# Performance work log

Measured on AMD Instinct MI355X. Metric: run time of the kernel, lower is better.

The kernel has to match this reference:

```python
import jax, jax.numpy as jnp
import numpy as np

H = 4      # attention heads
C = 64     # hidden_dim per head
GAT_SLOPE = 0.2   # PyG GATConv leaky_relu negative_slope
ACT_SLOPE = 0.01  # nn.LeakyReLU / F.leaky_relu default


def gat_layer(x, src, dst, W, a_src, a_dst, b, n):
    # x: [n, F_in] -> h: [n, H, C]
    h = (x @ W).reshape(n, H, C)
    al_s = jnp.einsum('nhc,hc->nh', h, a_src)  # [n, H]
    al_d = jnp.einsum('nhc,hc->nh', h, a_dst)
    e = jax.nn.leaky_relu(al_s[src] + al_d[dst], GAT_SLOPE)  # [E, H]
    # segment softmax over destination nodes (self-loops ensure non-empty segments)
    m = jax.ops.segment_max(e, dst, num_segments=n)
    p = jnp.exp(e - m[dst])
    s = jax.ops.segment_sum(p, dst, num_segments=n)
    alpha = p / s[dst]
    out = jax.ops.segment_sum(h[src] * alpha[:, :, None], dst, num_segments=n)  # [n, H, C]
    return out.reshape(n, H * C) + b


def setup_inputs() -> dict:
    key = jax.random.key(0)
    ks = jax.random.split(key, 24)
    N, E = 102400, 409600
    F_IN, F_OUT = 80, 80
    HC = H * C
    RIN, RHID, ROUT = 60, 512, 60
    def g(k, shape, scale):
        return (jax.random.normal(k, shape, dtype=jnp.float32) * scale)
    inp = {
        'x': g(ks[0], (N, F_IN), 1.0),
        'edge_index': jax.random.randint(ks[1], (2, E), 0, N, dtype=jnp.int64),
        'root_ctx_norm': g(ks[2], (4096, RIN), 1.0),
        'W0': g(ks[3], (F_IN, HC), 0.1), 'a_src0': g(ks[4], (H, C), 0.1), 'a_dst0': g(ks[5], (H, C), 0.1), 'b0': jnp.zeros((HC,), jnp.float32),
        'W1': g(ks[6], (HC, HC), 0.06), 'a_src1': g(ks[7], (H, C), 0.1), 'a_dst1': g(ks[8], (H, C), 0.1), 'b1': jnp.zeros((HC,), jnp.float32),
        'W2': g(ks[9], (HC, HC), 0.06), 'a_src2': g(ks[10], (H, C), 0.1), 'a_dst2': g(ks[11], (H, C), 0.1), 'b2': jnp.zeros((HC,), jnp.float32),
        'fc_w': g(ks[12], (HC, F_OUT), 0.06), 'fc_b': jnp.zeros((F_OUT,), jnp.float32),
        'r_w1': g(ks[13], (RIN, RHID), 0.1), 'r_b1': jnp.zeros((RHID,), jnp.float32),
        'r_w2': g(ks[14], (RHID, RHID), 0.04), 'r_b2': jnp.zeros((RHID,), jnp.float32),
        'r_w3': g(ks[15], (RHID, ROUT), 0.04), 'r_b3': jnp.zeros((ROUT,), jnp.float32),
    }
    return inp


def reference(x, edge_index, root_ctx_norm,
              W0, a_src0, a_dst0, b0,
              W1, a_src1, a_dst1, b1,
              W2, a_src2, a_dst2, b2,
              fc_w, fc_b, r_w1, r_b1, r_w2, r_b2, r_w3, r_b3):
    n = x.shape[0]
    loops = jnp.arange(n, dtype=edge_index.dtype)
    src = jnp.concatenate([edge_index[0], loops])  # PyG add_self_loops=True
    dst = jnp.concatenate([edge_index[1], loops])
    h = gat_layer(x, src, dst, W0, a_src0, a_dst0, b0, n)
    h = jax.nn.leaky_relu(h, ACT_SLOPE)  # dropout is identity in eval
    h = gat_layer(h, src, dst, W1, a_src1, a_dst1, b1, n)
    h = jax.nn.leaky_relu(h, ACT_SLOPE)
    h = gat_layer(h, src, dst, W2, a_src2, a_dst2, b2, n)
    rot = h @ fc_w + fc_b
    r = jax.nn.leaky_relu(root_ctx_norm @ r_w1 + r_b1, ACT_SLOPE)
    r = jax.nn.leaky_relu(r @ r_w2 + r_b2, ACT_SLOPE)
    root_norm = r @ r_w3 + r_b3
    return rot, root_norm
```

## Files before the change

kernel.cpp:

```cpp
#include <hip/hip_runtime.h>
#include <hip/hip_bf16.h>


#define GAT_SLOPE 0.2f
#define ACT_SLOPE 0.01f

typedef unsigned short ushort_t;
typedef __attribute__((ext_vector_type(8))) short bf16x8;
typedef __attribute__((ext_vector_type(8))) unsigned short ushort8v;
typedef __attribute__((ext_vector_type(4))) float floatx4;

__device__ __forceinline__ float lrelu(float x, float s) {
    return fmaxf(x, s * x);
}

__device__ __forceinline__ ushort_t f2bf(float f) {
    union { float f; unsigned u; } x; x.f = f;
    unsigned r = x.u + 0x7FFF + ((x.u >> 16) & 1);
    return (ushort_t)(r >> 16);
}

__device__ __forceinline__ float bf2f(ushort_t u) {
    union { unsigned u; float f; } x; x.u = ((unsigned)u) << 16;
    return x.f;
}

__global__ void detect_fmt(const int* __restrict__ raw, int nwords, int* flag) {
    __shared__ int nz;
    if (threadIdx.x == 0) nz = 0;
    __syncthreads();
    int lim = nwords < 4096 ? nwords : 4096;
    for (int i = threadIdx.x * 2 + 1; i < lim; i += 512)
        if (raw[i] != 0) atomicAdd(&nz, 1);
    __syncthreads();
    if (threadIdx.x == 0) *flag = (nz == 0) ? 1 : 0;
}

__global__ void zero2(int* __restrict__ a, int* __restrict__ b, int n) {
    int i = blockIdx.x * blockDim.x + threadIdx.x;
    if (i < n) { a[i] = 0; b[i] = 0; }
}

__global__ void convert_count(const int* __restrict__ raw, int E,
                              const int* __restrict__ flag,
                              int* __restrict__ idx32, int* __restrict__ counts) {
    int i = blockIdx.x * blockDim.x + threadIdx.x;
    if (i >= E) return;
    int f = *flag;
    int s = f ? raw[2 * i] : raw[i];
    int d = f ? raw[2 * (E + i)] : raw[E + i];
    idx32[i] = s;
    idx32[E + i] = d;
    atomicAdd(&counts[d], 1);
}

__global__ void scan_block(const int* __restrict__ counts, int* __restrict__ inc,
                           int* __restrict__ blockSums, int N) {
    __shared__ int sh[256];
    int i = blockIdx.x * 256 + threadIdx.x;
    int v = (i < N) ? counts[i] : 0;
    sh[threadIdx.x] = v;
    __syncthreads();
    for (int off = 1; off < 256; off <<= 1) {
        int t = (threadIdx.x >= off) ? sh[threadIdx.x - off] : 0;
        __syncthreads();
        sh[threadIdx.x] += t;
        __syncthreads();
    }
    if (i < N) inc[i] = sh[threadIdx.x];
    if (threadIdx.x == 255) blockSums[blockIdx.x] = sh[255];
}

__global__ void scan_sums(int* __restrict__ blockSums, int nb, int* __restrict__ row_ptr) {
    __shared__ int sh[512];
    int v = ((int)threadIdx.x < nb) ? blockSums[threadIdx.x] : 0;
    sh[threadIdx.x] = v;
    __syncthreads();
    for (int off = 1; off < 512; off <<= 1) {
        int t = (threadIdx.x >= off) ? sh[threadIdx.x - off] : 0;
        __syncthreads();
        sh[threadIdx.x] += t;
        __syncthreads();
    }
    if ((int)threadIdx.x < nb) blockSums[threadIdx.x] = sh[threadIdx.x];
    if (threadIdx.x == 0) row_ptr[0] = 0;
}

__global__ void scan_add(const int* __restrict__ inc, const int* __restrict__ blockSums,
                         int* __restrict__ row_ptr, int N) {
    int i = blockIdx.x * 256 + threadIdx.x;
    if (i < N) row_ptr[i + 1] = inc[i] + (blockIdx.x > 0 ? blockSums[blockIdx.x - 1] : 0);
}

__global__ void edge_fill(const int* __restrict__ src, const int* __restrict__ dst, int E,
                          const int* __restrict__ row_ptr, int* __restrict__ cursor,
                          int* __restrict__ col) {
    int i = blockIdx.x * blockDim.x + threadIdx.x;
    if (i < E) {
        int d = dst[i];
        int pos = row_ptr[d] + atomicAdd(&cursor[d], 1);
        col[pos] = src[i];
    }
}

__global__ void convert_padrow(const float* __restrict__ in, ushort_t* __restrict__ out,
                               int M, int Kr, int Kp) {
    int i = blockIdx.x * blockDim.x + threadIdx.x;
    if (i >= M * Kp) return;
    int r = i / Kp, c = i - r * Kp;
    out[i] = f2bf((c < Kr) ? in[(size_t)r * Kr + c] : 0.f);
}

struct WConv { const float* in; ushort_t* out; int Kp, Kr, N, Npad, blkOff; };
struct WConvArr { WConv e[7]; int n; };

__global__ void convert_w_multi(WConvArr a) {
    int b = blockIdx.x;
    int ei = 0;
    for (int k = 1; k < a.n; k++)
        if (b >= a.e[k].blkOff) ei = k;
    WConv w = a.e[ei];
    int i = (b - w.blkOff) * 256 + threadIdx.x;
    if (i >= w.Npad * w.Kp) return;
    int n = i / w.Kp, k = i - n * w.Kp;
    float v = (n < w.N && k < w.Kr) ? w.in[(size_t)k * w.N + n] : 0.f;
    w.out[i] = f2bf(v);
}

#define LOADR(tt)                                     \
    do {                                              \
        int k0_ = (tt) << 5;                          \
        rA0 = *(const ushort8v*)(gA0 + k0_);          \
        rA1 = *(const ushort8v*)(gA1 + k0_);          \
        rB0 = *(const ushort8v*)(gB0 + k0_);          \
        rB1 = *(const ushort8v*)(gB1 + k0_);          \
    } while (0)

#define WRITER(b)                                     \
    do {                                              \
        *(ushort8v*)(&As[b][wsl0]) = rA0;             \
        *(ushort8v*)(&As[b][wsl1]) = rA1;             \
        *(ushort8v*)(&Bs[b][wsl0]) = rB0;             \
        *(ushort8v*)(&Bs[b][wsl1]) = rB1;             \
    } while (0)

#define GEMM_PIPELINE(NT)                                                        \
    ushort8v rA0, rA1, rB0, rB1;                                                 \
    LOADR(0);                                                                    \
    WRITER(0);                                                                   \
    LOADR(1);                                                                    \
    asm volatile("s_waitcnt lgkmcnt(0)" ::: "memory");                           \
    __builtin_amdgcn_s_barrier();                                                \
    for (int kt = 0; kt < (NT); ++kt) {                                          \
        int b = kt & 1;                                                          \
        if (kt + 1 < (NT)) WRITER(b ^ 1);                                        \
        if (kt + 2 < (NT)) LOADR(kt + 2);                                        \
        bf16x8 af[4], bfv[4];                                                    \
        _Pragma("unroll")                                                        \
        for (int i = 0; i < 4; i++)                                              \
            af[i] = *(const bf16x8*)(&As[b][(wm + i * 16 + lrow) * 32            \
                                            + lquad * 8]);                       \
        _Pragma("unroll")                                                        \
        for (int j = 0; j < 4; j++)                                              \
            bfv[j] = *(const bf16x8*)(&Bs[b][(wn + j * 16 + lrow) * 32           \
                                             + lquad * 8]);                      \
        _Pragma("unroll")                                                        \
        for (int i = 0; i < 4; i++)                                              \
            _Pragma("unroll")                                                    \
            for (int j = 0; j < 4; j++)                                          \
                acc[i][j] = __builtin_amdgcn_mfma_f32_16x16x32_bf16(             \
                    af[i], bfv[j], acc[i][j], 0, 0, 0);                          \
        asm volatile("s_waitcnt lgkmcnt(0)" ::: "memory");                       \
        __builtin_amdgcn_s_barrier();                                            \
    }

__global__ __launch_bounds__(256) void gemm_gat(
    const ushort_t* __restrict__ A, const ushort_t* __restrict__ Bt,
    const float* __restrict__ a_src, const float* __restrict__ a_dst,
    ushort_t* __restrict__ Hbf, float* __restrict__ al_s, float* __restrict__ al_d,
    int K, int auxY,
    const ushort_t* __restrict__ xA, const ushort_t* __restrict__ xBt,
    const float* __restrict__ xBias, void* __restrict__ xC,
    int xN, int xK, int xGX, int xCnt, int xAct, float xSlope, int xOutBf) {
    __shared__ __align__(16) ushort_t As[2][128 * 32];
    __shared__ __align__(16) ushort_t Bs[2][128 * 32];
    int t = threadIdx.x;
    int wave = t >> 6, lane = t & 63;
    int wm = (wave >> 1) << 6;
    int wn = (wave & 1) << 6;
    int lrow = lane & 15, lquad = lane >> 4;
    const int wsl0 = (wave * 64 + lane) * 8;
    const int wsl1 = (256 + wave * 64 + lane) * 8;
    int c0 = wave * 64 + lane;
    int c1 = 256 + c0;

    floatx4 acc[4][4];
#pragma unroll
    for (int i = 0; i < 4; i++)
#pragma unroll
        for (int j = 0; j < 4; j++) acc[i][j] = (floatx4){0.f, 0.f, 0.f, 0.f};

    if ((int)blockIdx.y >= auxY) {
        int rowBase = (blockIdx.y - auxY) << 7;
        int colBase = blockIdx.x << 7;
        const ushort_t* gA0 = A + (size_t)(rowBase + (c0 >> 2)) * K + ((c0 & 3) << 3);
        const ushort_t* gB0 = Bt + (size_t)(colBase + (c0 >> 2)) * K + ((c0 & 3) << 3);
        const ushort_t* gA1 = A + (size_t)(rowBase + (c1 >> 2)) * K + ((c1 & 3) << 3);
        const ushort_t* gB1 = Bt + (size_t)(colBase + (c1 >> 2)) * K + ((c1 & 3) << 3);
        const int nt = K >> 5;
        GEMM_PIPELINE(nt);

        int head = (colBase + wn) >> 6;
        float avs[4], avd[4];
#pragma unroll
        for (int j = 0; j < 4; j++) {
            avs[j] = a_src[head * 64 + j * 16 + lrow];
            avd[j] = a_dst[head * 64 + j * 16 + lrow];
        }
#pragma unroll
        for (int i = 0; i < 4; i++) {
#pragma unroll
            for (int r = 0; r < 4; r++) {
                float ps = 0.f, pd = 0.f;
#pragma unroll
                for (int j = 0; j < 4; j++) {
                    ps += acc[i][j][r] * avs[j];
                    pd += acc[i][j][r] * avd[j];
                }
#pragma unroll
                for (int off = 1; off < 16; off <<= 1) {
                    ps += __shfl_xor(ps, off);
                    pd += __shfl_xor(pd, off);
                }
                if (lrow == 0) {
                    int gr = rowBase + wm + i * 16 + lquad * 4 + r;
                    al_s[gr * 4 + head] = ps;
                    al_d[gr * 4 + head] = pd;
                }
            }
            int grb = rowBase + wm + i * 16 + lquad * 4;
#pragma unroll
            for (int j = 0; j < 4; j++) {
                int gc = colBase + wn + j * 16 + lrow;
#pragma unroll
                for (int r = 0; r < 4; r++)
                    Hbf[(size_t)(grb + r) * 256 + gc] = f2bf(acc[i][j][r]);
            }
        }
    } else {
        int id = blockIdx.y * 2 + blockIdx.x;
        if (id >= xCnt) return;
        int bxp = id % xGX, byp = id / xGX;
        int rowBase = byp << 7;
        int colBase = bxp << 7;
        const ushort_t* gA0 = xA + (size_t)(rowBase + (c0 >> 2)) * xK + ((c0 & 3) << 3);
        const ushort_t* gB0 = xBt + (size_t)(colBase + (c0 >> 2)) * xK + ((c0 & 3) << 3);
        const ushort_t* gA1 = xA + (size_t)(rowBase + (c1 >> 2)) * xK + ((c1 & 3) << 3);
        const ushort_t* gB1 = xBt + (size_t)(colBase + (c1 >> 2)) * xK + ((c1 & 3) << 3);
        const int nt = xK >> 5;
        GEMM_PIPELINE(nt);

#pragma unroll
        for (int i = 0; i < 4; i++) {
            int gr = rowBase + wm + i * 16 + lquad * 4;
#pragma unroll
            for (int j = 0; j < 4; j++) {
                int gc = colBase + wn + j * 16 + lrow;
                if (gc >= xN) continue;
                float b = xBias ? xBias[gc] : 0.f;
#pragma unroll
                for (int r = 0; r < 4; r++) {
                    float v = acc[i][j][r] + b;
                    if (xAct) v = lrelu(v, xSlope);
                    if (xOutBf)
                        ((ushort_t*)xC)[(size_t)(gr + r) * xN + gc] = f2bf(v);
                    else
                        ((float*)xC)[(size_t)(gr + r) * xN + gc] = v;
                }
            }
        }
    }
}

__global__ __launch_bounds__(256) void gemm_plain(
    const ushort_t* __restrict__ A, const ushort_t* __restrict__ Bt,
    const float* __restrict__ bias, void* __restrict__ Cout,
    int M, int N, int K, int act, float slope, int outBf) {
    __shared__ __align__(16) ushort_t As[2][128 * 32];
    __shared__ __align__(16) ushort_t Bs[2][128 * 32];
    int t = threadIdx.x;
    int wave = t >> 6, lane = t & 63;
    int wm = (wave >> 1) << 6;
    int wn = (wave & 1) << 6;
    int rowBase = blockIdx.y << 7;
    int colBase = blockIdx.x << 7;
    int lrow = lane & 15, lquad = lane >> 4;
    floatx4 acc[4][4];
#pragma unroll
    for (int i = 0; i < 4; i++)
#pragma unroll
        for (int j = 0; j < 4; j++) acc[i][j] = (floatx4){0.f, 0.f, 0.f, 0.f};

    int c0 = wave * 64 + lane;
    const ushort_t* gA0 = A + (size_t)(rowBase + (c0 >> 2)) * K + ((c0 & 3) << 3);
    const ushort_t* gB0 = Bt + (size_t)(colBase + (c0 >> 2)) * K + ((c0 & 3) << 3);
    int c1 = 256 + c0;
    const ushort_t* gA1 = A + (size_t)(rowBase + (c1 >> 2)) * K + ((c1 & 3) << 3);
    const ushort_t* gB1 = Bt + (size_t)(colBase + (c1 >> 2)) * K + ((c1 & 3) << 3);
    const int wsl0 = (wave * 64 + lane) * 8;
    const int wsl1 = (256 + wave * 64 + lane) * 8;

    const int nt = K >> 5;
    GEMM_PIPELINE(nt);

#pragma unroll
    for (int i = 0; i < 4; i++) {
        int gr = rowBase + wm + i * 16 + lquad * 4;
#pragma unroll
        for (int j = 0; j < 4; j++) {
            int gc = colBase + wn + j * 16 + lrow;
            if (gc >= N) continue;
            float b = bias ? bias[gc] : 0.f;
#pragma unroll
            for (int r = 0; r < 4; r++) {
                float v = acc[i][j][r] + b;
                if (act) v = lrelu(v, slope);
                if (outBf)
                    ((ushort_t*)Cout)[(size_t)(gr + r) * N + gc] = f2bf(v);
                else
                    ((float*)Cout)[(size_t)(gr + r) * N + gc] = v;
            }
        }
    }
}

__global__ __launch_bounds__(256) void gat_agg(
    const ushort_t* __restrict__ h_bf, const float* __restrict__ al_s,
    const float* __restrict__ al_d, const int* __restrict__ row_ptr,
    const int* __restrict__ col, const float* __restrict__ bias,
    ushort_t* __restrict__ out_bf, int N, int act, float slope) {
    int wid = (blockIdx.x * 256 + threadIdx.x) >> 6;
    int lane = threadIdx.x & 63;
    int half = lane >> 5;
    int lane8 = lane & 31;
    int n = wid * 2 + half;
    if (n >= N) return;
    int head = lane8 >> 3;
    int idx4 = n * 4 + head;
    float ad = al_d[idx4];
    const ushort8v* h8 = (const ushort8v*)h_bf;
    float p = __expf(lrelu(al_s[idx4] + ad, GAT_SLOPE));
    ushort8v hv = h8[(size_t)n * 32 + lane8];
    float s = p;
    float acc[8];
#pragma unroll
    for (int c = 0; c < 8; c++) acc[c] = p * bf2f(hv[c]);
    int beg = row_ptr[n], end = row_ptr[n + 1];
    for (int i = beg; i < end; i += 4) {
        int cnt = end - i;
        int sn0 = col[i];
        int sn1 = (cnt > 1) ? col[i + 1] : sn0;
        int sn2 = (cnt > 2) ? col[i + 2] : sn0;
        int sn3 = (cnt > 3) ? col[i + 3] : sn0;
        ushort8v h0 = h8[(size_t)sn0 * 32 + lane8];
        ushort8v h1 = h8[(size_t)sn1 * 32 + lane8];
        ushort8v h2 = h8[(size_t)sn2 * 32 + lane8];
        ushort8v h3 = h8[(size_t)sn3 * 32 + lane8];
        float a0 = al_s[sn0 * 4 + head];
        float a1 = al_s[sn1 * 4 + head];
        float a2 = al_s[sn2 * 4 + head];
        float a3 = al_s[sn3 * 4 + head];
        float p0 = __expf(lrelu(a0 + ad, GAT_SLOPE));
#pragma unroll
        for (int c = 0; c < 8; c++) acc[c] += p0 * bf2f(h0[c]);
        s += p0;
        if (cnt > 1) {
            float p1 = __expf(lrelu(a1 + ad, GAT_SLOPE));
#pragma unroll
            for (int c = 0; c < 8; c++) acc[c] += p1 * bf2f(h1[c]);
            s += p1;
        }
        if (cnt > 2) {
            float p2 = __expf(lrelu(a2 + ad, GAT_SLOPE));
#pragma unroll
            for (int c = 0; c < 8; c++) acc[c] += p2 * bf2f(h2[c]);
            s += p2;
        }
        if (cnt > 3) {
            float p3 = __expf(lrelu(a3 + ad, GAT_SLOPE));
#pragma unroll
            for (int c = 0; c < 8; c++) acc[c] += p3 * bf2f(h3[c]);
            s += p3;
        }
    }
    float rs = 1.f / s;
    const float4* b4 = (const float4*)bias;
    float4 b0 = b4[lane8 * 2];
    float4 b1 = b4[lane8 * 2 + 1];
    float bv[8] = {b0.x, b0.y, b0.z, b0.w, b1.x, b1.y, b1.z, b1.w};
    ushort8v o;
#pragma unroll
    for (int c = 0; c < 8; c++) {
        float v = acc[c] * rs + bv[c];
        if (act) v = lrelu(v, slope);
        o[c] = f2bf(v);
    }
    ((ushort8v*)out_bf)[(size_t)n * 32 + lane8] = o;
}

extern "C" void kernel_launch(void* const* d_in, const int* in_sizes, int n_in,
                              void* d_out, int out_size, void* d_ws, size_t ws_size,
                              hipStream_t stream) {
    const float* x        = (const float*)d_in[0];
    const int*   rawEdge  = (const int*)d_in[1];
    const float* rootCtx  = (const float*)d_in[2];
    const float* W[3]     = {(const float*)d_in[3], (const float*)d_in[7], (const float*)d_in[11]};
    const float* aS[3]    = {(const float*)d_in[4], (const float*)d_in[8], (const float*)d_in[12]};
    const float* aD[3]    = {(const float*)d_in[5], (const float*)d_in[9], (const float*)d_in[13]};
    const float* bb[3]    = {(const float*)d_in[6], (const float*)d_in[10], (const float*)d_in[14]};
    const float* fc_w     = (const float*)d_in[15];
    const float* fc_b     = (const float*)d_in[16];
    const float* r_w1     = (const float*)d_in[17];
    const float* r_b1     = (const float*)d_in[18];
    const float* r_w2     = (const float*)d_in[19];
    const float* r_b2     = (const float*)d_in[20];
    const float* r_w3     = (const float*)d_in[21];
    const float* r_b3     = (const float*)d_in[22];

    const int N  = in_sizes[0] / 80;
    const int E  = in_sizes[1] / 2;
    const int R  = in_sizes[2] / 60;
    const int N4 = N * 4;

    float* outRot  = (float*)d_out;
    float* outRoot = (float*)d_out + (size_t)N * 80;

    size_t off = 0;
    auto carve = [&](size_t bytes) -> void* {
        off = (off + 255) & ~(size_t)255;
        void* p = (char*)d_ws + off;
        off += bytes;
        return p;
    };
    int*      flag      = (int*)carve(4);
    int*      idx32     = (int*)carve((size_t)2 * E * 4);
    int*      counts    = (int*)carve((size_t)N * 4);
    int*      cursor    = (int*)carve((size_t)N * 4);
    int*      row_ptr   = (int*)carve((size_t)(N + 1) * 4);
    int*      incArr    = (int*)carve((size_t)N * 4);
    int*      blockSums = (int*)carve(512 * 4);
    int*      colArr    = (int*)carve((size_t)E * 4);
    float*    al_s      = (float*)carve((size_t)N4 * 4);
    float*    al_d      = (float*)carve((size_t)N4 * 4);
    ushort_t* h_bf      = (ushort_t*)carve((size_t)N * 256 * 2);
    ushort_t* agg_bf    = (ushort_t*)carve((size_t)N * 256 * 2);
    ushort_t* x_bf      = (ushort_t*)carve((size_t)N * 96 * 2);
    ushort_t* rc_bf     = (ushort_t*)carve((size_t)R * 64 * 2);
    ushort_t* t1_bf     = (ushort_t*)carve((size_t)R * 512 * 2);
    ushort_t* t2_bf     = (ushort_t*)carve((size_t)R * 512 * 2);
    ushort_t* Wt0       = (ushort_t*)carve((size_t)256 * 96 * 2);
    ushort_t* Wt1       = (ushort_t*)carve((size_t)256 * 256 * 2);
    ushort_t* Wt2       = (ushort_t*)carve((size_t)256 * 256 * 2);
    ushort_t* fcWt      = (ushort_t*)carve((size_t)128 * 256 * 2);
    ushort_t* rW1t      = (ushort_t*)carve((size_t)512 * 64 * 2);
    ushort_t* rWt2      = (ushort_t*)carve((size_t)512 * 512 * 2);
    ushort_t* rWt3      = (ushort_t*)carve((size_t)128 * 512 * 2);

    const int nb = (N + 255) / 256;
    dim3 blk(256);

    detect_fmt<<<1, 256, 0, stream>>>(rawEdge, 2 * E, flag);
    zero2<<<(N + 255) / 256, blk, 0, stream>>>(counts, cursor, N);
    convert_count<<<(E + 255) / 256, blk, 0, stream>>>(rawEdge, E, flag, idx32, counts);
    const int* srcArr = idx32;
    const int* dstArr = idx32 + E;
    scan_block<<<nb, 256, 0, stream>>>(counts, incArr, blockSums, N);
    scan_sums<<<1, 512, 0, stream>>>(blockSums, nb, row_ptr);
    scan_add<<<nb, 256, 0, stream>>>(incArr, blockSums, row_ptr, N);
    edge_fill<<<(E + 255) / 256, blk, 0, stream>>>(srcArr, dstArr, E, row_ptr, cursor, colArr);

    {
        WConvArr wa;
        auto mk = [&](int i, const float* in, ushort_t* out, int Kp, int Kr, int Nn, int Npad,
                      int blkOff) {
            wa.e[i] = WConv{in, out, Kp, Kr, Nn, Npad, blkOff};
        };
        int boff = 0;
        auto nblk = [](int Npad, int Kp) { return (Npad * Kp + 255) / 256; };
        mk(0, W[0], Wt0, 96, 80, 256, 256, boff);   boff += nblk(256, 96);
        mk(1, W[1], Wt1, 256, 256, 256, 256, boff); boff += nblk(256, 256);
        mk(2, W[2], Wt2, 256, 256, 256, 256, boff); boff += nblk(256, 256);
        mk(3, fc_w, fcWt, 256, 256, 80, 128, boff); boff += nblk(128, 256);
        mk(4, r_w1, rW1t, 64, 60, 512, 512, boff);  boff += nblk(512, 64);
        mk(5, r_w2, rWt2, 512, 512, 512, 512, boff); boff += nblk(512, 512);
        mk(6, r_w3, rWt3, 512, 512, 60, 128, boff);  boff += nblk(128, 512);
        wa.n = 7;
        convert_w_multi<<<boff, blk, 0, stream>>>(wa);
    }
    convert_padrow<<<(N * 96 + 255) / 256, blk, 0, stream>>>(x, x_bf, N, 80, 96);
    convert_padrow<<<(R * 64 + 255) / 256, blk, 0, stream>>>(rootCtx, rc_bf, R, 60, 64);

    const int aggBlocks = (N / 2 + 3) / 4;
    const int yMain = N / 128;
    const ushort_t* curA = x_bf;
    int curK = 96;
    const int mlpGY = R / 128;
    for (int l = 0; l < 3; l++) {
        const ushort_t* xA  = (l == 0) ? rc_bf : (l == 1 ? t1_bf : t2_bf);
        const ushort_t* xBt = (l == 0) ? rW1t : (l == 1 ? rWt2 : rWt3);
        const float*    xB  = (l == 0) ? r_b1 : (l == 1 ? r_b2 : r_b3);
        void*           xC  = (l == 0) ? (void*)t1_bf : (l == 1 ? (void*)t2_bf : (void*)outRoot);
        int xN   = (l == 2) ? 60 : 512;
        int xK   = (l == 0) ? 64 : 512;
        int xGX  = (l == 2) ? 1 : 4;
        int xCnt = xGX * mlpGY;
        int xAct = (l == 2) ? 0 : 1;
        int xOutBf = (l == 2) ? 0 : 1;
        int auxY = (xCnt + 1) / 2;
        dim3 g1(2, yMain + auxY);
        gemm_gat<<<g1, blk, 0, stream>>>(curA, l == 0 ? Wt0 : (l == 1 ? Wt1 : Wt2),
                                         aS[l], aD[l], h_bf, al_s, al_d,
                                         curK, auxY,
                                         xA, xBt, xB, xC,
                                         xN, xK, xGX, xCnt, xAct, ACT_SLOPE, xOutBf);
        int act = (l < 2) ? 1 : 0;
        gat_agg<<<aggBlocks, blk, 0, stream>>>(h_bf, al_s, al_d, row_ptr,
                                               colArr, bb[l], agg_bf, N,
                                               act, ACT_SLOPE);
        curA = agg_bf;
        curK = 256;
    }

    {
        dim3 g(1, N / 128);
        gemm_plain<<<g, blk, 0, stream>>>(agg_bf, fcWt, fc_b, outRot, N, 80, 256,
                                          0, 0.f, 0);
    }
}
```

Before: 469.4 us.

## Fuse graph preprocessing and weight conversion into one cooperative kernel

Replaces the separate format-detect, zeroing, count, three-stage scan, edge fill and bf16 conversion kernels with a single cooperative kernel that uses grid-wide syncs between phases. This is meant to remove per-launch overhead and the idle gaps between many small dependent kernels. In exchange, the work runs on a fixed 1024-block grid with grid-stride loops and pays grid-sync latency. It also relies on all blocks being co-resident.

```diff
diff --git a/kernel.cpp b/kernel.cpp
--- a/kernel.cpp
+++ b/kernel.cpp
@@ -1,5 +1,8 @@
 #include <hip/hip_runtime.h>
 #include <hip/hip_bf16.h>
+#include <hip/hip_cooperative_groups.h>
+
+namespace cg = cooperative_groups;
 
 
 #define GAT_SLOPE 0.2f
@@ -25,106 +28,129 @@
     return x.f;
 }
 
-__global__ void detect_fmt(const int* __restrict__ raw, int nwords, int* flag) {
-    __shared__ int nz;
-    if (threadIdx.x == 0) nz = 0;
-    __syncthreads();
-    int lim = nwords < 4096 ? nwords : 4096;
-    for (int i = threadIdx.x * 2 + 1; i < lim; i += 512)
-        if (raw[i] != 0) atomicAdd(&nz, 1);
-    __syncthreads();
-    if (threadIdx.x == 0) *flag = (nz == 0) ? 1 : 0;
-}
-
-__global__ void zero2(int* __restrict__ a, int* __restrict__ b, int n) {
-    int i = blockIdx.x * blockDim.x + threadIdx.x;
-    if (i < n) { a[i] = 0; b[i] = 0; }
-}
-
-__global__ void convert_count(const int* __restrict__ raw, int E,
-                              const int* __restrict__ flag,
-                              int* __restrict__ idx32, int* __restrict__ counts) {
-    int i = blockIdx.x * blockDim.x + threadIdx.x;
-    if (i >= E) return;
-    int f = *flag;
-    int s = f ? raw[2 * i] : raw[i];
-    int d = f ? raw[2 * (E + i)] : raw[E + i];
-    idx32[i] = s;
-    idx32[E + i] = d;
-    atomicAdd(&counts[d], 1);
-}
-
-__global__ void scan_block(const int* __restrict__ counts, int* __restrict__ inc,
-                           int* __restrict__ blockSums, int N) {
+struct WConv { const float* in; ushort_t* out; int Kp, Kr, N, Npad; };
+
+struct PreArgs {
+    const int* rawEdge;
+    int E, N, R;
+    int* flag;
+    int* idx32;
+    int* counts;
+    int* cursor;
+    int* row_ptr;
+    int* incArr;
+    int* blockSums;
+    int* colArr;
+    const float* x;  ushort_t* x_bf;
+    const float* rc; ushort_t* rc_bf;
+    WConv w[7];
+};
+
+__global__ void preamble_all(PreArgs a) {
+    cg::grid_group grid = cg::this_grid();
+    const int tid  = blockIdx.x * blockDim.x + threadIdx.x;
+    const int nthr = gridDim.x * blockDim.x;
     __shared__ int sh[256];
-    int i = blockIdx.x * 256 + threadIdx.x;
-    int v = (i < N) ? counts[i] : 0;
-    sh[threadIdx.x] = v;
-    __syncthreads();
-    for (int off = 1; off < 256; off <<= 1) {
-        int t = (threadIdx.x >= off) ? sh[threadIdx.x - off] : 0;
+
+    for (int i = tid; i < a.N; i += nthr) { a.counts[i] = 0; a.cursor[i] = 0; }
+    {
+        int tot = a.N * 96;
+        for (int i = tid; i < tot; i += nthr) {
+            int r = i / 96, c = i - r * 96;
+            a.x_bf[i] = f2bf((c < 80) ? a.x[(size_t)r * 80 + c] : 0.f);
+        }
+    }
+    {
+        int tot = a.R * 64;
+        for (int i = tid; i < tot; i += nthr) {
+            int r = i / 64, c = i - r * 64;
+            a.rc_bf[i] = f2bf((c < 60) ? a.rc[(size_t)r * 60 + c] : 0.f);
+        }
+    }
+    for (int e = 0; e < 7; e++) {
+        WConv w = a.w[e];
+        int tot = w.Npad * w.Kp;
+        for (int i = tid; i < tot; i += nthr) {
+            int n = i / w.Kp, k = i - n * w.Kp;
+            float v = (n < w.N && k < w.Kr) ? w.in[(size_t)k * w.N + n] : 0.f;
+            w.out[i] = f2bf(v);
+        }
+    }
+    if (blockIdx.x == 0) {
+        __shared__ int nz;
+        if (threadIdx.x == 0) nz = 0;
         __syncthreads();
-        sh[threadIdx.x] += t;
+        int lim = 2 * a.E < 4096 ? 2 * a.E : 4096;
+        for (int i = threadIdx.x * 2 + 1; i < lim; i += 512)
+            if (a.rawEdge[i] != 0) atomicAdd(&nz, 1);
         __syncthreads();
-    }
-    if (i < N) inc[i] = sh[threadIdx.x];
-    if (threadIdx.x == 255) blockSums[blockIdx.x] = sh[255];
-}
-
-__global__ void scan_sums(int* __restrict__ blockSums, int nb, int* __restrict__ row_ptr) {
-    __shared__ int sh[512];
-    int v = ((int)threadIdx.x < nb) ? blockSums[threadIdx.x] : 0;
-    sh[threadIdx.x] = v;
-    __syncthreads();
-    for (int off = 1; off < 512; off <<= 1) {
-        int t = (threadIdx.x >= off) ? sh[threadIdx.x - off] : 0;
+        if (threadIdx.x == 0) *a.flag = (nz == 0) ? 1 : 0;
+    }
+    grid.sync();
+
+    {
+        int fmt = *a.flag;
+        for (int i = tid; i < a.E; i += nthr) {
+            int s = fmt ? a.rawEdge[2 * i] : a.rawEdge[i];
+            int d = fmt ? a.rawEdge[2 * (a.E + i)] : a.rawEdge[a.E + i];
+            a.idx32[i] = s;
+            a.idx32[a.E + i] = d;
+            atomicAdd(&a.counts[d], 1);
+        }
+    }
+    grid.sync();
+
+    const int nb = (a.N + 255) / 256;
+    for (int ch = blockIdx.x; ch < nb; ch += gridDim.x) {
+        int i = ch * 256 + threadIdx.x;
+        int v = (i < a.N) ? a.counts[i] : 0;
+        sh[threadIdx.x] = v;
         __syncthreads();
-        sh[threadIdx.x] += t;
+        for (int off = 1; off < 256; off <<= 1) {
+            int t2 = (threadIdx.x >= off) ? sh[threadIdx.x - off] : 0;
+            __syncthreads();
+            sh[threadIdx.x] += t2;
+            __syncthreads();
+        }
+        if (i < a.N) a.incArr[i] = sh[threadIdx.x];
+        if (threadIdx.x == 255) a.blockSums[ch] = sh[255];
         __syncthreads();
     }
-    if ((int)threadIdx.x < nb) blockSums[threadIdx.x] = sh[threadIdx.x];
-    if (threadIdx.x == 0) row_ptr[0] = 0;
-}
-
-__global__ void scan_add(const int* __restrict__ inc, const int* __restrict__ blockSums,
-                         int* __restrict__ row_ptr, int N) {
-    int i = blockIdx.x * 256 + threadIdx.x;
-    if (i < N) row_ptr[i + 1] = inc[i] + (blockIdx.x > 0 ? blockSums[blockIdx.x - 1] : 0);
-}
-
-__global__ void edge_fill(const int* __restrict__ src, const int* __restrict__ dst, int E,
-                          const int* __restrict__ row_ptr, int* __restrict__ cursor,
-                          int* __restrict__ col) {
-    int i = blockIdx.x * blockDim.x + threadIdx.x;
-    if (i < E) {
-        int d = dst[i];
-        int pos = row_ptr[d] + atomicAdd(&cursor[d], 1);
-        col[pos] = src[i];
-    }
-}
-
-__global__ void convert_padrow(const float* __restrict__ in, ushort_t* __restrict__ out,
-                               int M, int Kr, int Kp) {
-    int i = blockIdx.x * blockDim.x + threadIdx.x;
-    if (i >= M * Kp) return;
-    int r = i / Kp, c = i - r * Kp;
-    out[i] = f2bf((c < Kr) ? in[(size_t)r * Kr + c] : 0.f);
-}
-
-struct WConv { const float* in; ushort_t* out; int Kp, Kr, N, Npad, blkOff; };
-struct WConvArr { WConv e[7]; int n; };
-
-__global__ void convert_w_multi(WConvArr a) {
-    int b = blockIdx.x;
-    int ei = 0;
-    for (int k = 1; k < a.n; k++)
-        if (b >= a.e[k].blkOff) ei = k;
-    WConv w = a.e[ei];
-    int i = (b - w.blkOff) * 256 + threadIdx.x;
-    if (i >= w.Npad * w.Kp) return;
-    int n = i / w.Kp, k = i - n * w.Kp;
-    float v = (n < w.N && k < w.Kr) ? w.in[(size_t)k * w.N + n] : 0.f;
-    w.out[i] = f2bf(v);
+    grid.sync();
+
+    if (blockIdx.x == 0) {
+        int carry = 0;
+        for (int base = 0; base < nb; base += 256) {
+            int idx = base + threadIdx.x;
+            int v = (idx < nb) ? a.blockSums[idx] : 0;
+            sh[threadIdx.x] = v;
+            __syncthreads();
+            for (int off = 1; off < 256; off <<= 1) {
+                int t2 = (threadIdx.x >= off) ? sh[threadIdx.x - off] : 0;
+                __syncthreads();
+                sh[threadIdx.x] += t2;
+                __syncthreads();
+            }
+            if (idx < nb) a.blockSums[idx] = sh[threadIdx.x] + carry;
+            int chunkTot = sh[255];
+            __syncthreads();
+            carry += chunkTot;
+        }
+    }
+    grid.sync();
+
+    for (int i = tid; i < a.N; i += nthr) {
+        int ch = i >> 8;
+        a.row_ptr[i + 1] = a.incArr[i] + (ch > 0 ? a.blockSums[ch - 1] : 0);
+    }
+    if (tid == 0) a.row_ptr[0] = 0;
+    grid.sync();
+
+    for (int i = tid; i < a.E; i += nthr) {
+        int d = a.idx32[a.E + i];
+        int pos = a.row_ptr[d] + atomicAdd(&a.cursor[d], 1);
+        a.colArr[pos] = a.idx32[i];
+    }
 }
 
 #define LOADR(tt)                                     \
@@ -464,41 +490,28 @@
     ushort_t* fcWt      = (ushort_t*)carve((size_t)128 * 256 * 2);
     ushort_t* rW1t      = (ushort_t*)carve((size_t)512 * 64 * 2);
     ushort_t* rWt2      = (ushort_t*)carve((size_t)512 * 512 * 2);
-    ushort_t* rWt3      = (ushort_t*)carve((size_t)128 * 512 * 2);
-
-    const int nb = (N + 255) / 256;
+    ushort_t* rWt3     = (ushort_t*)carve((size_t)128 * 512 * 2);
+
     dim3 blk(256);
 
-    detect_fmt<<<1, 256, 0, stream>>>(rawEdge, 2 * E, flag);
-    zero2<<<(N + 255) / 256, blk, 0, stream>>>(counts, cursor, N);
-    convert_count<<<(E + 255) / 256, blk, 0, stream>>>(rawEdge, E, flag, idx32, counts);
-    const int* srcArr = idx32;
-    const int* dstArr = idx32 + E;
-    scan_block<<<nb, 256, 0, stream>>>(counts, incArr, blockSums, N);
-    scan_sums<<<1, 512, 0, stream>>>(blockSums, nb, row_ptr);
-    scan_add<<<nb, 256, 0, stream>>>(incArr, blockSums, row_ptr, N);
-    edge_fill<<<(E + 255) / 256, blk, 0, stream>>>(srcArr, dstArr, E, row_ptr, cursor, colArr);
-
     {
-        WConvArr wa;
-        auto mk = [&](int i, const float* in, ushort_t* out, int Kp, int Kr, int Nn, int Npad,
-                      int blkOff) {
-            wa.e[i] = WConv{in, out, Kp, Kr, Nn, Npad, blkOff};
-        };
-        int boff = 0;
-        auto nblk = [](int Npad, int Kp) { return (Npad * Kp + 255) / 256; };
-        mk(0, W[0], Wt0, 96, 80, 256, 256, boff);   boff += nblk(256, 96);
-        mk(1, W[1], Wt1, 256, 256, 256, 256, boff); boff += nblk(256, 256);
-        mk(2, W[2], Wt2, 256, 256, 256, 256, boff); boff += nblk(256, 256);
-        mk(3, fc_w, fcWt, 256, 256, 80, 128, boff); boff += nblk(128, 256);
-        mk(4, r_w1, rW1t, 64, 60, 512, 512, boff);  boff += nblk(512, 64);
-        mk(5, r_w2, rWt2, 512, 512, 512, 512, boff); boff += nblk(512, 512);
-        mk(6, r_w3, rWt3, 512, 512, 60, 128, boff);  boff += nblk(128, 512);
-        wa.n = 7;
-        convert_w_multi<<<boff, blk, 0, stream>>>(wa);
-    }
-    convert_padrow<<<(N * 96 + 255) / 256, blk, 0, stream>>>(x, x_bf, N, 80, 96);
-    convert_padrow<<<(R * 64 + 255) / 256, blk, 0, stream>>>(rootCtx, rc_bf, R, 60, 64);
+        PreArgs pa;
+        pa.rawEdge = rawEdge; pa.E = E; pa.N = N; pa.R = R;
+        pa.flag = flag; pa.idx32 = idx32; pa.counts = counts; pa.cursor = cursor;
+        pa.row_ptr = row_ptr; pa.incArr = incArr; pa.blockSums = blockSums;
+        pa.colArr = colArr;
+        pa.x = x; pa.x_bf = x_bf; pa.rc = rootCtx; pa.rc_bf = rc_bf;
+        pa.w[0] = WConv{W[0], Wt0, 96, 80, 256, 256};
+        pa.w[1] = WConv{W[1], Wt1, 256, 256, 256, 256};
+        pa.w[2] = WConv{W[2], Wt2, 256, 256, 256, 256};
+        pa.w[3] = WConv{fc_w, fcWt, 256, 256, 80, 128};
+        pa.w[4] = WConv{r_w1, rW1t, 64, 60, 512, 512};
+        pa.w[5] = WConv{r_w2, rWt2, 512, 512, 512, 512};
+        pa.w[6] = WConv{r_w3, rWt3, 512, 512, 60, 128};
+        void* kargs[] = { (void*)&pa };
+        hipLaunchCooperativeKernel((void*)preamble_all, dim3(1024), blk,
+                                   kargs, 0, stream);
+    }
 
     const int aggBlocks = (N / 2 + 3) / 4;
     const int yMain = N / 128;
```

Measured after the change: 1.038 ms. +121.1%, slower.
